# Performance work log

Hardware: AMD Instinct MI355X
Metric: run time of the kernel (lower is better)

Reference implementation:

```python
import jax, jax.numpy as jnp
import numpy as np

B, N, M, DIM = 64, 512, 512, 8
BANDWIDTH = 0.1  # Sakoe-Chiba band (fraction of normalized path deviation)


def setup_inputs() -> dict:
    key = jax.random.key(0)
    kx, ky = jax.random.split(key)
    X = jax.random.normal(kx, (B, N, DIM), dtype=jnp.float32)
    Y = jax.random.normal(ky, (B, M, DIM), dtype=jnp.float32)
    return {"X": X, "Y": Y}


def _sqdist(x, y):
    # ||x_i - y_j||^2 per timestep pair -> [B, N, M]; gram-matrix form avoids
    # materializing the [B,N,M,D] broadcast the torch code expands.
    x2 = jnp.sum(x * x, axis=-1)[:, :, None]
    y2 = jnp.sum(y * y, axis=-1)[:, None, :]
    xy = jnp.einsum('bnd,bmd->bnm', x, y)
    return x2 + y2 - 2.0 * xy


def _dtw(D, bandwidth):
    # Anti-diagonal wavefront min-plus DP, matching compute_dtw / compute_dtw_cuda.
    Bz, n, m = D.shape
    bw = max(bandwidth, 1.0 / (n - 1), 1.0 / (m - 1))  # same clamp as original
    inv_n, inv_m = 1.0 / (n - 1), 1.0 / (m - 1)
    ii = jnp.arange(n)

    def step(carry, d):
        rm2, rm1 = carry  # diagonals d-2 and d-1, each [B, n] indexed by i
        j = d - ii  # column index on diagonal d
        jc = jnp.clip(j, 0, m - 1)
        inside = (j >= 0) & (j < m)
        in_band = jnp.abs(ii * inv_n - j * inv_m) <= bw
        valid = inside & in_band
        Dd = D[:, ii, jc]  # [B, n] cost along this diagonal
        pad = jnp.full((Bz, 1), jnp.inf, D.dtype)
        r0 = jnp.concatenate([pad, rm2[:, :-1]], axis=1)  # R[i-1, j-1]
        r0 = jnp.where((d == 0) & (ii == 0), 0.0, r0)      # R[-1,-1] = 0 seed
        r1 = jnp.concatenate([pad, rm1[:, :-1]], axis=1)  # R[i-1, j]
        r2 = rm1                                           # R[i, j-1]
        # tie-break priority r0 >= r1 >= r2 matches the original argmin order
        rmin = jnp.minimum(jnp.minimum(r0, r1), r2)
        r = jnp.where(valid, Dd + rmin, jnp.inf)
        return (rm1, r), r

    init = (jnp.full((Bz, n), jnp.inf, D.dtype),
            jnp.full((Bz, n), jnp.inf, D.dtype))
    _, diags = jax.lax.scan(step, init, jnp.arange(n + m - 1))  # [n+m-1, B, n]
    loss = diags[-1, :, n - 1]  # R[n-1, m-1] per batch
    # Unskew diagonals back to the padded R matrix the torch op returns.
    jj = jnp.arange(m)
    Rcore = diags[ii[:, None] + jj[None, :], :, ii[:, None]]  # [n, m, B]
    Rcore = jnp.moveaxis(Rcore, -1, 0)  # [B, n, m]
    Rfull = jnp.full((Bz, n + 2, m + 2), jnp.inf, D.dtype)
    Rfull = Rfull.at[:, 0, 0].set(0.0).at[:, 1:n + 1, 1:m + 1].set(Rcore)
    return loss, Rfull


def reference(X, Y):
    D = _sqdist(X, Y)
    loss, R = _dtw(D, BANDWIDTH)
    return (loss, R)
```

## Files before the change

### kernel.cpp

```cpp
#include <hip/hip_runtime.h>

#define BATCH 64
#define NN 512
#define DIMS 8
#define RDIM 514
#define WB 51
#define NDIAG (2 * NN - 1)
#define DPAD 1024
#define NG4 256
#define CHUNK 64
#define NCHUNK 16
#define GRP 16
#define NGRP 64

__device__ __forceinline__ constexpr int lo_of(int d) {
  int v = (d - (WB - 1)) >> 1;
  int w = d - (NN - 1);
  v = v > w ? v : w;
  return v > 0 ? v : 0;
}
__device__ __forceinline__ int hi_of(int d) {
  return min(min(d, NN - 1), (d + WB) >> 1);
}

__device__ __forceinline__ float dpp_shr1(float x, float old) {
  return __int_as_float(__builtin_amdgcn_update_dpp(
      __float_as_int(old), __float_as_int(x), 0x138, 0xF, 0xF, false));
}
__device__ __forceinline__ float dpp_shl1(float x, float old) {
  return __int_as_float(__builtin_amdgcn_update_dpp(
      __float_as_int(old), __float_as_int(x), 0x130, 0xF, 0xF, false));
}

__device__ __forceinline__ float dval(const float* __restrict__ Xb,
                                      const float* __restrict__ Yb,
                                      int ic, int jc) {
  const float4* xp = (const float4*)(Xb + (size_t)ic * DIMS);
  const float4* yp = (const float4*)(Yb + (size_t)jc * DIMS);
  float4 xa = xp[0], xb2 = xp[1];
  float4 ya = yp[0], yb2 = yp[1];
  float x2 = xa.x * xa.x + xa.y * xa.y + xa.z * xa.z + xa.w * xa.w +
             xb2.x * xb2.x + xb2.y * xb2.y + xb2.z * xb2.z + xb2.w * xb2.w;
  float y2 = ya.x * ya.x + ya.y * ya.y + ya.z * ya.z + ya.w * ya.w +
             yb2.x * yb2.x + yb2.y * yb2.y + yb2.z * yb2.z + yb2.w * yb2.w;
  float dot = xa.x * ya.x + xa.y * ya.y + xa.z * ya.z + xa.w * ya.w +
              xb2.x * yb2.x + xb2.y * yb2.y + xb2.z * yb2.z + xb2.w * yb2.w;
  return (x2 + y2) - 2.0f * dot;
}

__global__ __launch_bounds__(256) void dpre_kernel(const float* __restrict__ X,
                                                   const float* __restrict__ Y,
                                                   float4* __restrict__ Dws4) {
  const int b = blockIdx.x & 63;
  const int ng = (blockIdx.x >> 6) * 4 + (threadIdx.x >> 6);
  const int lane = threadIdx.x & 63;
  const float INF = __builtin_inff();
  const float* __restrict__ Xb = X + (size_t)b * NN * DIMS;
  const float* __restrict__ Yb = Y + (size_t)b * NN * DIMS;
  float o[4];
#pragma unroll
  for (int k = 0; k < 4; ++k) {
    const int n = 4 * ng + k;
    const int lon = lo_of(n);
    const int i = lon + lane;
    const bool valid = (i <= hi_of(n)) && (n < NDIAG);
    const int ic = min(i, NN - 1);
    const int jc = min(max(n - ic, 0), NN - 1);
    float D = dval(Xb, Yb, ic, jc);
    o[k] = valid ? D : INF;
  }
  Dws4[((size_t)b * NG4 + ng) * 64 + lane] = make_float4(o[0], o[1], o[2], o[3]);
}

#define BODY_STEP(qm, n)                                                    \
      const int lon = lo_of(n);                                             \
      const int d1 = lon - lo_of((n) - 1);                                  \
      const int d2 = lon - lo_of((n) - 2);                                  \
      float s_shl = dpp_shl1(r_d, INF);                                     \
      float s_shr = dpp_shr1(r_d, INF);                                     \
      float tt = d1 ? s_shl : s_shr;                                        \
      float vc = (d2 == 0) ? shm_shr : ((d2 == 1) ? r_dm1 : shm_shl);       \
      float r = (qm) + fminf(fminf(r_d, tt), vc);                           \
      r_dm1 = r_d; shm_shl = s_shl; shm_shr = s_shr; r_d = r;

#define STEADY_STEP(qm, m)                                                  \
      float tt = ((m & 1) == 0) ? dpp_shl1(r_d, INF) : dpp_shr1(r_d, INF);  \
      float r = (qm) + fminf(fminf(r_d, tt), r_dm1);                        \
      r_dm1 = r_d; r_d = r;

__global__ __launch_bounds__(64, 1) void dtw_chain_kernel(const float4* __restrict__ Dws4,
                                                          float* __restrict__ ckpt,
                                                          float* __restrict__ out) {
  __shared__ float ckls[NGRP * 2 * 64];
  const int b = blockIdx.x;
  const int lane = threadIdx.x;
  const float INF = __builtin_inff();
  const float4* __restrict__ Db4 = Dws4 + (size_t)b * NG4 * 64 + lane;

  float qA[CHUNK], qB[CHUNK], qC[CHUNK];

#define LOAD_CHUNK(q, cRt)                                                  \
  { _Pragma("unroll")                                                       \
    for (int mg = 0; mg < 16; ++mg) {                                       \
      float4 v = Db4[(size_t)((cRt) * 16 + mg) * 64];                       \
      (q)[4 * mg + 0] = v.x; (q)[4 * mg + 1] = v.y;                         \
      (q)[4 * mg + 2] = v.z; (q)[4 * mg + 3] = v.w;                         \
    } }

#define CKPT16(g)                                                           \
  { ckls[((g) * 2 + 0) * 64 + lane] = r_d;                                  \
    ckls[((g) * 2 + 1) * 64 + lane] = r_dm1; }

  float r_d = INF, r_dm1 = INF, shm_shl = INF;
  float shm_shr = (lane == 0) ? 0.0f : INF;

  LOAD_CHUNK(qA, 0)
  LOAD_CHUNK(qB, 1)
  LOAD_CHUNK(qC, 2)
  {
#pragma unroll
    for (int m = 0; m < CHUNK; ++m) {
      if ((m & 15) == 0) { CKPT16(m >> 4) }
      BODY_STEP(qA[m], 0 + m)
    }
  }
  LOAD_CHUNK(qA, 3)
#pragma unroll 1
  for (int c = 1; c <= 10; c += 3) {
    {
#pragma unroll
      for (int m = 0; m < CHUNK; ++m) {
        if ((m & 15) == 0) { CKPT16(c * 4 + (m >> 4)) }
        STEADY_STEP(qB[m], m)
      }
    }
    LOAD_CHUNK(qB, c + 3)
    {
#pragma unroll
      for (int m = 0; m < CHUNK; ++m) {
        if ((m & 15) == 0) { CKPT16((c + 1) * 4 + (m >> 4)) }
        STEADY_STEP(qC[m], m)
      }
    }
    LOAD_CHUNK(qC, c + 4)
    {
#pragma unroll
      for (int m = 0; m < CHUNK; ++m) {
        if ((m & 15) == 0) { CKPT16((c + 2) * 4 + (m >> 4)) }
        STEADY_STEP(qA[m], m)
      }
    }
    LOAD_CHUNK(qA, c + 5)
  }
  {
#pragma unroll
    for (int m = 0; m < CHUNK; ++m) {
      if ((m & 15) == 0) { CKPT16(13 * 4 + (m >> 4)) }
      STEADY_STEP(qB[m], m)
    }
  }
  {
#pragma unroll
    for (int m = 0; m < CHUNK; ++m) {
      if ((m & 15) == 0) { CKPT16(14 * 4 + (m >> 4)) }
      STEADY_STEP(qC[m], m)
    }
  }
  {
#pragma unroll
    for (int m = 0; m < CHUNK; ++m) {
      if ((m & 15) == 0) { CKPT16(15 * 4 + (m >> 4)) }
      BODY_STEP(qA[m], 960 + m)
    }
  }

  if (lane == 0) out[b] = r_dm1;

  {
    const float4* s4 = (const float4*)ckls;
    float4* d4 = (float4*)(ckpt + (size_t)b * (NGRP * 2) * 64);
    for (int k = lane; k < NGRP * 2 * 16; k += 64) d4[k] = s4[k];
  }
#undef LOAD_CHUNK
#undef CKPT16
}

__global__ __launch_bounds__(256) void dtw_par_kernel(const float4* __restrict__ Dws4,
                                                      const float* __restrict__ ckpt,
                                                      float* __restrict__ out) {
  __shared__ float T[CHUNK][65];
  const int b = blockIdx.x & 63;
  const int cc = blockIdx.x >> 6;
  const int t = threadIdx.x;
  const int wave = t >> 6, lane = t & 63;
  const float INF = __builtin_inff();
  const int dlo = cc * CHUNK;

  float* __restrict__ Rfull = out + BATCH + (size_t)b * RDIM * RDIM;
  if (cc == 0 && t == 0) Rfull[0] = 0.0f;

  {
    const int g = cc * 4 + wave;
    const int n0 = g * GRP;
    const float4* __restrict__ Db4 = Dws4 + ((size_t)b * NG4 + g * 4) * 64 + lane;
    float q[GRP];
#pragma unroll
    for (int mg = 0; mg < 4; ++mg) {
      float4 v = Db4[(size_t)mg * 64];
      q[4 * mg + 0] = v.x; q[4 * mg + 1] = v.y;
      q[4 * mg + 2] = v.z; q[4 * mg + 3] = v.w;
    }

    const float* __restrict__ ckb =
        ckpt + ((size_t)b * (NGRP * 2) + g * 2) * 64 + lane;
    float r_d = ckb[0];
    float r_dm1 = ckb[64];
    float shm_shl = dpp_shl1(r_dm1, INF);
    float shm_shr = dpp_shr1(r_dm1, INF);
    if (g == 0) shm_shr = (lane == 0) ? 0.0f : INF;

    int lop = lo_of(n0 - 1), lopp = lo_of(n0 - 2);
#pragma unroll
    for (int m = 0; m < GRP; ++m) {
      const int n = n0 + m;
      const int lon = lo_of(n);
      const int d1 = lon - lop;
      const int d2 = lon - lopp;
      float s_shl = dpp_shl1(r_d, INF);
      float s_shr = dpp_shr1(r_d, INF);
      float tt = d1 ? s_shl : s_shr;
      float vc = (d2 == 0) ? shm_shr : ((d2 == 1) ? r_dm1 : shm_shl);
      float r = q[m] + fminf(fminf(r_d, tt), vc);
      T[wave * GRP + m][lane] = r;
      r_dm1 = r_d; shm_shl = s_shl; shm_shr = s_shr; r_d = r;
      lopp = lop; lop = lon;
    }
  }
  __syncthreads();

  const int dhi1 = min(dlo + CHUNK - 1, NDIAG - 1);
  const int rlo = lo_of(dlo);
  const int rhi = hi_of(dhi1);
  for (int i = rlo + wave; i <= rhi; i += 4) {
    const int j0 = max(max(i - WB, dlo - i), 0);
    const int j1 = min(min(i + WB, dhi1 - i), NN - 1);
    const int j = j0 + lane;
    if (j <= j1) {
      const int n = i + j;
      const int dd = n - dlo;
      const int l2 = i - lo_of(n);
      Rfull[(size_t)(i + 1) * RDIM + (j + 1)] = T[dd][l2];
    }
  }
}

__global__ __launch_bounds__(256) void dtw_fb_kernel(const float* __restrict__ X,
                                                     const float* __restrict__ Y,
                                                     float* __restrict__ out) {
  __shared__ float xsT[DIMS][NN];
  __shared__ float ysT[DIMS][NN];
  __shared__ float x2s[NN];
  __shared__ float y2s[NN];
  __shared__ float ring[2][CHUNK][64];

  const int b = blockIdx.x;
  const int t = threadIdx.x;
  const float INF = __builtin_inff();

  {
    const float4* Xg = (const float4*)(X + (size_t)b * NN * DIMS);
    const float4* Yg = (const float4*)(Y + (size_t)b * NN * DIMS);
    for (int r = t; r < NN; r += 256) {
      float4 a0 = Xg[2 * r], a1 = Xg[2 * r + 1];
      xsT[0][r] = a0.x; xsT[1][r] = a0.y; xsT[2][r] = a0.z; xsT[3][r] = a0.w;
      xsT[4][r] = a1.x; xsT[5][r] = a1.y; xsT[6][r] = a1.z; xsT[7][r] = a1.w;
      x2s[r] = a0.x * a0.x + a0.y * a0.y + a0.z * a0.z + a0.w * a0.w +
               a1.x * a1.x + a1.y * a1.y + a1.z * a1.z + a1.w * a1.w;
      float4 c0 = Yg[2 * r], c1 = Yg[2 * r + 1];
      ysT[0][r] = c0.x; ysT[1][r] = c0.y; ysT[2][r] = c0.z; ysT[3][r] = c0.w;
      ysT[4][r] = c1.x; ysT[5][r] = c1.y; ysT[6][r] = c1.z; ysT[7][r] = c1.w;
      y2s[r] = c0.x * c0.x + c0.y * c0.y + c0.z * c0.z + c0.w * c0.w +
               c1.x * c1.x + c1.y * c1.y + c1.z * c1.z + c1.w * c1.w;
    }
  }
  __syncthreads();

  float* __restrict__ Rfull = out + BATCH + (size_t)b * RDIM * RDIM;
  if (t == 64) Rfull[0] = 0.0f;

  const int lane = t & 63;
  float r_d = INF, r_dm1 = INF;
  int lop = 0, lopp = 0;
  float Dcur = 0.0f;
  if (t < 64) {
    int i0 = min(lane, NN - 1);
    int j0 = max(0, min(0 - i0, NN - 1));
    float dot = xsT[0][i0] * ysT[0][j0] + xsT[1][i0] * ysT[1][j0] +
                xsT[2][i0] * ysT[2][j0] + xsT[3][i0] * ysT[3][j0] +
                xsT[4][i0] * ysT[4][j0] + xsT[5][i0] * ysT[5][j0] +
                xsT[6][i0] * ysT[6][j0] + xsT[7][i0] * ysT[7][j0];
    Dcur = (x2s[i0] + y2s[j0]) - 2.0f * dot;
  }

  for (int c = 0; c <= NCHUNK; ++c) {
    if (t < 64 && c < NCHUNK) {
      const int dlo = c * CHUNK;
      const int dhi = min(dlo + CHUNK, NDIAG);
      for (int n = dlo; n < dhi; ++n) {
        const int lon = lo_of(n), hin = hi_of(n);
        const int d1 = lon - lop;
        const int d2 = lon - lopp;
        const int sa = lane + d1;
        const int sb = sa - 1;
        const int sc = lane + d2 - 1;
        float va = __shfl(r_d, sa);   va = (sa < 64) ? va : INF;
        float vb = __shfl(r_d, sb);   vb = (sb >= 0) ? vb : INF;
        float vc = __shfl(r_dm1, sc); vc = (sc >= 0 && sc < 64) ? vc : INF;
        float rmin = fminf(fminf(vc, vb), va);
        if (n == 0) rmin = (lane == 0) ? 0.0f : INF;
        float r = Dcur + rmin;
        if (lane > hin - lon) r = INF;
        ring[c & 1][n - dlo][lane] = r;
        const int lon1 = lo_of(n + 1);
        int ii = min(lon1 + lane, NN - 1);
        int jj = n + 1 - ii; jj = max(0, min(jj, NN - 1));
        float dot = xsT[0][ii] * ysT[0][jj] + xsT[1][ii] * ysT[1][jj] +
                    xsT[2][ii] * ysT[2][jj] + xsT[3][ii] * ysT[3][jj] +
                    xsT[4][ii] * ysT[4][jj] + xsT[5][ii] * ysT[5][jj] +
                    xsT[6][ii] * ysT[6][jj] + xsT[7][ii] * ysT[7][jj];
        Dcur = (x2s[ii] + y2s[jj]) - 2.0f * dot;
        r_dm1 = r_d; r_d = r;
        lopp = lop; lop = lon;
      }
    } else if (t >= 64 && c >= 1) {
      const int dlo = (c - 1) * CHUNK;
      const int dhi = min(dlo + CHUNK, NDIAG);
      const int nslots = (dhi - dlo) * 64;
      const int buf = (c - 1) & 1;
      for (int s = t - 64; s < nslots; s += 192) {
        const int dd = s >> 6, l2 = s & 63;
        const int n = dlo + dd;
        const int lon = lo_of(n);
        const int i = lon + l2;
        if (i <= hi_of(n)) {
          Rfull[(size_t)(i + 1) * RDIM + (n - i + 1)] = ring[buf][dd][l2];
        }
      }
    }
    __syncthreads();
  }

  if (t == 0) out[b] = r_d;
}

extern "C" void kernel_launch(void* const* d_in, const int* in_sizes, int n_in,
                              void* d_out, int out_size, void* d_ws, size_t ws_size,
                              hipStream_t stream) {
  const float* X = (const float*)d_in[0];
  const float* Y = (const float*)d_in[1];
  float* out = (float*)d_out;

  const size_t nD = (size_t)BATCH * DPAD * 64;
  const size_t nC = (size_t)BATCH * NGRP * 2 * 64;
  if (ws_size >= (nD + nC) * sizeof(float)) {
    float4* Dws4 = (float4*)d_ws;
    float* ckpt = (float*)d_ws + nD;
    dpre_kernel<<<(BATCH * NG4) / 4, 256, 0, stream>>>(X, Y, Dws4);
    dtw_chain_kernel<<<BATCH, 64, 0, stream>>>(Dws4, ckpt, out);
    dtw_par_kernel<<<BATCH * NCHUNK, 256, 0, stream>>>(Dws4, ckpt, out);
  } else {
    dtw_fb_kernel<<<BATCH, 256, 0, stream>>>(X, Y, out);
  }
}
```

Baseline: 40.33 us.

## Fuse D precompute, serial DTW chain, and parallel replay into one kernel

Replaces the three-kernel pipeline with a single per-batch kernel: all four waves first compute the banded cost diagonals into workspace, then wave 0 runs the serial anti-diagonal chain saving checkpoints in shared memory, then all waves replay chunks from those checkpoints and scatter R into the output. This removes two kernel launches and the global checkpoint buffer. In exchange, precompute and output writing run on only 64 blocks instead of thousands, which limits memory-level parallelism for the large R write. Two-slot register buffering replaces the three-slot one in the chain.

```diff
diff --git a/kernel.cpp b/kernel.cpp
--- a/kernel.cpp
+++ b/kernel.cpp
@@ -48,30 +48,6 @@
   return (x2 + y2) - 2.0f * dot;
 }
 
-__global__ __launch_bounds__(256) void dpre_kernel(const float* __restrict__ X,
-                                                   const float* __restrict__ Y,
-                                                   float4* __restrict__ Dws4) {
-  const int b = blockIdx.x & 63;
-  const int ng = (blockIdx.x >> 6) * 4 + (threadIdx.x >> 6);
-  const int lane = threadIdx.x & 63;
-  const float INF = __builtin_inff();
-  const float* __restrict__ Xb = X + (size_t)b * NN * DIMS;
-  const float* __restrict__ Yb = Y + (size_t)b * NN * DIMS;
-  float o[4];
-#pragma unroll
-  for (int k = 0; k < 4; ++k) {
-    const int n = 4 * ng + k;
-    const int lon = lo_of(n);
-    const int i = lon + lane;
-    const bool valid = (i <= hi_of(n)) && (n < NDIAG);
-    const int ic = min(i, NN - 1);
-    const int jc = min(max(n - ic, 0), NN - 1);
-    float D = dval(Xb, Yb, ic, jc);
-    o[k] = valid ? D : INF;
-  }
-  Dws4[((size_t)b * NG4 + ng) * 64 + lane] = make_float4(o[0], o[1], o[2], o[3]);
-}
-
 #define BODY_STEP(qm, n)                                                    \
       const int lon = lo_of(n);                                             \
       const int d1 = lon - lo_of((n) - 1);                                  \
@@ -88,18 +64,46 @@
       float r = (qm) + fminf(fminf(r_d, tt), r_dm1);                        \
       r_dm1 = r_d; r_d = r;
 
-__global__ __launch_bounds__(64, 1) void dtw_chain_kernel(const float4* __restrict__ Dws4,
-                                                          float* __restrict__ ckpt,
-                                                          float* __restrict__ out) {
+__global__ __launch_bounds__(256, 1) void dtw_all_kernel(const float* __restrict__ X,
+                                                         const float* __restrict__ Y,
+                                                         float4* __restrict__ Dws4,
+                                                         float* __restrict__ out) {
   __shared__ float ckls[NGRP * 2 * 64];
+  __shared__ float T[4][CHUNK][65];
   const int b = blockIdx.x;
-  const int lane = threadIdx.x;
+  const int wave = threadIdx.x >> 6, lane = threadIdx.x & 63;
   const float INF = __builtin_inff();
-  const float4* __restrict__ Db4 = Dws4 + (size_t)b * NG4 * 64 + lane;
-
-  float qA[CHUNK], qB[CHUNK], qC[CHUNK];
-
-#define LOAD_CHUNK(q, cRt)                                                  \
+
+  const float* __restrict__ Xb = X + (size_t)b * NN * DIMS;
+  const float* __restrict__ Yb = Y + (size_t)b * NN * DIMS;
+  float4* __restrict__ Db4w = Dws4 + (size_t)b * NG4 * 64;
+  float* __restrict__ Rfull = out + BATCH + (size_t)b * RDIM * RDIM;
+  if (threadIdx.x == 0) Rfull[0] = 0.0f;
+
+  for (int k = 0; k < 64; ++k) {
+    const int ng = wave * 64 + k;
+    float o[4];
+#pragma unroll
+    for (int kk = 0; kk < 4; ++kk) {
+      const int n = 4 * ng + kk;
+      const int lon = lo_of(n);
+      const int i = lon + lane;
+      const bool valid = (i <= hi_of(n)) && (n < NDIAG);
+      const int ic = min(i, NN - 1);
+      const int jc = min(max(n - ic, 0), NN - 1);
+      float D = dval(Xb, Yb, ic, jc);
+      o[kk] = valid ? D : INF;
+    }
+    Db4w[(size_t)ng * 64 + lane] = make_float4(o[0], o[1], o[2], o[3]);
+  }
+  __threadfence();
+  __syncthreads();
+
+  if (wave == 0) {
+    const float4* __restrict__ Db4 = Db4w + lane;
+    float qA[CHUNK], qB[CHUNK];
+
+#define LOAD4(q, cRt)                                                       \
   { _Pragma("unroll")                                                       \
     for (int mg = 0; mg < 16; ++mg) {                                       \
       float4 v = Db4[(size_t)((cRt) * 16 + mg) * 64];                       \
@@ -111,146 +115,105 @@
   { ckls[((g) * 2 + 0) * 64 + lane] = r_d;                                  \
     ckls[((g) * 2 + 1) * 64 + lane] = r_dm1; }
 
-  float r_d = INF, r_dm1 = INF, shm_shl = INF;
-  float shm_shr = (lane == 0) ? 0.0f : INF;
-
-  LOAD_CHUNK(qA, 0)
-  LOAD_CHUNK(qB, 1)
-  LOAD_CHUNK(qC, 2)
-  {
-#pragma unroll
-    for (int m = 0; m < CHUNK; ++m) {
-      if ((m & 15) == 0) { CKPT16(m >> 4) }
-      BODY_STEP(qA[m], 0 + m)
-    }
-  }
-  LOAD_CHUNK(qA, 3)
+    float r_d = INF, r_dm1 = INF, shm_shl = INF;
+    float shm_shr = (lane == 0) ? 0.0f : INF;
+
+    LOAD4(qA, 0)
+    LOAD4(qB, 1)
+    {
+#pragma unroll
+      for (int m = 0; m < CHUNK; ++m) {
+        if ((m & 15) == 0) { CKPT16(m >> 4) }
+        BODY_STEP(qA[m], 0 + m)
+      }
+    }
+    LOAD4(qA, 2)
 #pragma unroll 1
-  for (int c = 1; c <= 10; c += 3) {
+    for (int c = 1; c <= 14; ++c) {
+      if (c & 1) {
+#pragma unroll
+        for (int m = 0; m < CHUNK; ++m) {
+          if ((m & 15) == 0) { CKPT16(c * 4 + (m >> 4)) }
+          STEADY_STEP(qB[m], m)
+        }
+        if (c + 2 <= 15) LOAD4(qB, c + 2)
+      } else {
+#pragma unroll
+        for (int m = 0; m < CHUNK; ++m) {
+          if ((m & 15) == 0) { CKPT16(c * 4 + (m >> 4)) }
+          STEADY_STEP(qA[m], m)
+        }
+        if (c + 2 <= 15) LOAD4(qA, c + 2)
+      }
+    }
     {
 #pragma unroll
       for (int m = 0; m < CHUNK; ++m) {
-        if ((m & 15) == 0) { CKPT16(c * 4 + (m >> 4)) }
-        STEADY_STEP(qB[m], m)
-      }
-    }
-    LOAD_CHUNK(qB, c + 3)
-    {
-#pragma unroll
-      for (int m = 0; m < CHUNK; ++m) {
-        if ((m & 15) == 0) { CKPT16((c + 1) * 4 + (m >> 4)) }
-        STEADY_STEP(qC[m], m)
-      }
-    }
-    LOAD_CHUNK(qC, c + 4)
-    {
-#pragma unroll
-      for (int m = 0; m < CHUNK; ++m) {
-        if ((m & 15) == 0) { CKPT16((c + 2) * 4 + (m >> 4)) }
-        STEADY_STEP(qA[m], m)
-      }
-    }
-    LOAD_CHUNK(qA, c + 5)
-  }
-  {
-#pragma unroll
-    for (int m = 0; m < CHUNK; ++m) {
-      if ((m & 15) == 0) { CKPT16(13 * 4 + (m >> 4)) }
-      STEADY_STEP(qB[m], m)
-    }
-  }
-  {
-#pragma unroll
-    for (int m = 0; m < CHUNK; ++m) {
-      if ((m & 15) == 0) { CKPT16(14 * 4 + (m >> 4)) }
-      STEADY_STEP(qC[m], m)
-    }
-  }
-  {
-#pragma unroll
-    for (int m = 0; m < CHUNK; ++m) {
-      if ((m & 15) == 0) { CKPT16(15 * 4 + (m >> 4)) }
-      BODY_STEP(qA[m], 960 + m)
-    }
-  }
-
-  if (lane == 0) out[b] = r_dm1;
-
-  {
-    const float4* s4 = (const float4*)ckls;
-    float4* d4 = (float4*)(ckpt + (size_t)b * (NGRP * 2) * 64);
-    for (int k = lane; k < NGRP * 2 * 16; k += 64) d4[k] = s4[k];
-  }
-#undef LOAD_CHUNK
+        if ((m & 15) == 0) { CKPT16(15 * 4 + (m >> 4)) }
+        BODY_STEP(qB[m], 960 + m)
+      }
+    }
+    if (lane == 0) out[b] = r_dm1;
+#undef LOAD4
 #undef CKPT16
-}
-
-__global__ __launch_bounds__(256) void dtw_par_kernel(const float4* __restrict__ Dws4,
-                                                      const float* __restrict__ ckpt,
-                                                      float* __restrict__ out) {
-  __shared__ float T[CHUNK][65];
-  const int b = blockIdx.x & 63;
-  const int cc = blockIdx.x >> 6;
-  const int t = threadIdx.x;
-  const int wave = t >> 6, lane = t & 63;
-  const float INF = __builtin_inff();
-  const int dlo = cc * CHUNK;
-
-  float* __restrict__ Rfull = out + BATCH + (size_t)b * RDIM * RDIM;
-  if (cc == 0 && t == 0) Rfull[0] = 0.0f;
-
-  {
-    const int g = cc * 4 + wave;
-    const int n0 = g * GRP;
-    const float4* __restrict__ Db4 = Dws4 + ((size_t)b * NG4 + g * 4) * 64 + lane;
-    float q[GRP];
-#pragma unroll
-    for (int mg = 0; mg < 4; ++mg) {
-      float4 v = Db4[(size_t)mg * 64];
-      q[4 * mg + 0] = v.x; q[4 * mg + 1] = v.y;
-      q[4 * mg + 2] = v.z; q[4 * mg + 3] = v.w;
-    }
-
-    const float* __restrict__ ckb =
-        ckpt + ((size_t)b * (NGRP * 2) + g * 2) * 64 + lane;
-    float r_d = ckb[0];
-    float r_dm1 = ckb[64];
-    float shm_shl = dpp_shl1(r_dm1, INF);
-    float shm_shr = dpp_shr1(r_dm1, INF);
-    if (g == 0) shm_shr = (lane == 0) ? 0.0f : INF;
-
-    int lop = lo_of(n0 - 1), lopp = lo_of(n0 - 2);
-#pragma unroll
-    for (int m = 0; m < GRP; ++m) {
-      const int n = n0 + m;
-      const int lon = lo_of(n);
-      const int d1 = lon - lop;
-      const int d2 = lon - lopp;
-      float s_shl = dpp_shl1(r_d, INF);
-      float s_shr = dpp_shr1(r_d, INF);
-      float tt = d1 ? s_shl : s_shr;
-      float vc = (d2 == 0) ? shm_shr : ((d2 == 1) ? r_dm1 : shm_shl);
-      float r = q[m] + fminf(fminf(r_d, tt), vc);
-      T[wave * GRP + m][lane] = r;
-      r_dm1 = r_d; shm_shl = s_shl; shm_shr = s_shr; r_d = r;
-      lopp = lop; lop = lon;
-    }
   }
   __syncthreads();
 
-  const int dhi1 = min(dlo + CHUNK - 1, NDIAG - 1);
-  const int rlo = lo_of(dlo);
-  const int rhi = hi_of(dhi1);
-  for (int i = rlo + wave; i <= rhi; i += 4) {
-    const int j0 = max(max(i - WB, dlo - i), 0);
-    const int j1 = min(min(i + WB, dhi1 - i), NN - 1);
-    const int j = j0 + lane;
-    if (j <= j1) {
-      const int n = i + j;
-      const int dd = n - dlo;
-      const int l2 = i - lo_of(n);
-      Rfull[(size_t)(i + 1) * RDIM + (j + 1)] = T[dd][l2];
-    }
+  for (int rr = 0; rr < 4; ++rr) {
+    const int cc = wave + rr * 4;
+    const int dlo = cc * CHUNK;
+    for (int grp = 0; grp < 4; ++grp) {
+      const int g = cc * 4 + grp;
+      const int n0 = g * GRP;
+      const float4* __restrict__ Db4 = Db4w + (size_t)(g * 4) * 64 + lane;
+      float q[GRP];
+#pragma unroll
+      for (int mg = 0; mg < 4; ++mg) {
+        float4 v = Db4[(size_t)mg * 64];
+        q[4 * mg + 0] = v.x; q[4 * mg + 1] = v.y;
+        q[4 * mg + 2] = v.z; q[4 * mg + 3] = v.w;
+      }
+      float r_d = ckls[(g * 2 + 0) * 64 + lane];
+      float r_dm1 = ckls[(g * 2 + 1) * 64 + lane];
+      float shm_shl = dpp_shl1(r_dm1, INF);
+      float shm_shr = dpp_shr1(r_dm1, INF);
+      if (g == 0) shm_shr = (lane == 0) ? 0.0f : INF;
+
+      int lop = lo_of(n0 - 1), lopp = lo_of(n0 - 2);
+#pragma unroll
+      for (int m = 0; m < GRP; ++m) {
+        const int n = n0 + m;
+        const int lon = lo_of(n);
+        const int d1 = lon - lop;
+        const int d2 = lon - lopp;
+        float s_shl = dpp_shl1(r_d, INF);
+        float s_shr = dpp_shr1(r_d, INF);
+        float tt = d1 ? s_shl : s_shr;
+        float vc = (d2 == 0) ? shm_shr : ((d2 == 1) ? r_dm1 : shm_shl);
+        float r = q[m] + fminf(fminf(r_d, tt), vc);
+        T[wave][grp * GRP + m][lane] = r;
+        r_dm1 = r_d; shm_shl = s_shl; shm_shr = s_shr; r_d = r;
+        lopp = lop; lop = lon;
+      }
+    }
+    __builtin_amdgcn_s_waitcnt(0);
+    __builtin_amdgcn_wave_barrier();
+
+    const int dhi1 = min(dlo + CHUNK - 1, NDIAG - 1);
+    const int rlo = lo_of(dlo);
+    const int rhi = hi_of(dhi1);
+    for (int i = rlo; i <= rhi; ++i) {
+      const int j0 = max(max(i - WB, dlo - i), 0);
+      const int j1 = min(min(i + WB, dhi1 - i), NN - 1);
+      const int j = j0 + lane;
+      if (j <= j1) {
+        const int n = i + j;
+        const int dd = n - dlo;
+        const int l2 = i - lo_of(n);
+        Rfull[(size_t)(i + 1) * RDIM + (j + 1)] = T[wave][dd][l2];
+      }
+    }
+    __builtin_amdgcn_wave_barrier();
   }
 }
 
@@ -361,13 +324,9 @@
   float* out = (float*)d_out;
 
   const size_t nD = (size_t)BATCH * DPAD * 64;
-  const size_t nC = (size_t)BATCH * NGRP * 2 * 64;
-  if (ws_size >= (nD + nC) * sizeof(float)) {
+  if (ws_size >= nD * sizeof(float)) {
     float4* Dws4 = (float4*)d_ws;
-    float* ckpt = (float*)d_ws + nD;
-    dpre_kernel<<<(BATCH * NG4) / 4, 256, 0, stream>>>(X, Y, Dws4);
-    dtw_chain_kernel<<<BATCH, 64, 0, stream>>>(Dws4, ckpt, out);
-    dtw_par_kernel<<<BATCH * NCHUNK, 256, 0, stream>>>(Dws4, ckpt, out);
+    dtw_all_kernel<<<BATCH, 256, 0, stream>>>(X, Y, Dws4, out);
   } else {
     dtw_fb_kernel<<<BATCH, 256, 0, stream>>>(X, Y, out);
   }
```

Result: slower. 111.7 us (+177.0%).
